# Performance work log

Hardware: AMD Instinct MI355X
Metric: run time of the kernel (lower is better)

## Reference

```python
import jax, jax.numpy as jnp
import numpy as np

GROUPS = 8
HEADS = 8
EPS = 1e-5


def group_norm(x, w, b, groups=GROUPS, eps=EPS):
    # x: [B, C, D, H, W]
    B, C, D, H, W = x.shape
    xg = x.reshape(B, groups, C // groups, D, H, W)
    mu = xg.mean(axis=(2, 3, 4, 5), keepdims=True)
    var = xg.var(axis=(2, 3, 4, 5), keepdims=True)
    xn = ((xg - mu) / jnp.sqrt(var + eps)).reshape(B, C, D, H, W)
    return xn * w[None, :, None, None, None] + b[None, :, None, None, None]


def conv1x1(x, w, b):
    # 1x1x1 Conv3d == channel-mixing GEMM. w: [Cout, Cin], x: [B, Cin, D, H, W]
    y = jnp.einsum('oc,bcdhw->bodhw', w, x)
    return y + b[None, :, None, None, None]


def setup_inputs() -> dict:
    key = jax.random.key(0)
    ks = jax.random.split(key, 8)
    C, CTX = 512, 512
    B, D, H, W = 1, 16, 16, 16
    x = jax.random.normal(ks[0], (B, C, D, H, W), dtype=jnp.float32)
    context = jax.random.normal(ks[1], (B, CTX, D, H, W), dtype=jnp.float32)
    return {
        'x': x,
        'context': context,
        'norm_w': jnp.ones((C,), jnp.float32),
        'norm_b': jnp.zeros((C,), jnp.float32),
        'normc_w': jnp.ones((CTX,), jnp.float32),
        'normc_b': jnp.zeros((CTX,), jnp.float32),
        'q_w': jax.random.normal(ks[2], (C, C), jnp.float32) * 0.02,
        'q_b': jnp.zeros((C,), jnp.float32),
        'kv_w': jax.random.normal(ks[3], (2 * C, CTX), jnp.float32) * 0.02,
        'kv_b': jnp.zeros((2 * C,), jnp.float32),
        'proj_w': jax.random.normal(ks[4], (C, C), jnp.float32) * 0.02,
        'proj_b': jnp.zeros((C,), jnp.float32),
    }


def _split_heads(t, heads):
    # [B, (h c), D, H, W] -> [B, h, S, c] with S = D*H*W
    B, C, D, H, W = t.shape
    return t.reshape(B, heads, C // heads, D * H * W).transpose(0, 1, 3, 2)


def reference(x, context, norm_w, norm_b, normc_w, normc_b,
              q_w, q_b, kv_w, kv_b, proj_w, proj_b):
    B, C, D, H, W = x.shape
    h = group_norm(x, norm_w, norm_b)
    c = group_norm(context, normc_w, normc_b)
    q = conv1x1(h, q_w, q_b)
    kv = conv1x1(c, kv_w, kv_b)
    k, v = jnp.split(kv, 2, axis=1)
    q = _split_heads(q, HEADS)   # [B, h, S, c]
    k = _split_heads(k, HEADS)
    v = _split_heads(v, HEADS)
    scale = (C // HEADS) ** (-0.5)
    logits = jnp.einsum('bhqc,bhkc->bhqk', q, k) * scale
    attn = jax.nn.softmax(logits, axis=-1)
    out = jnp.einsum('bhqk,bhkc->bhqc', attn, v)
    # [B, h, S, c] -> [B, (h c), D, H, W]
    out = out.transpose(0, 1, 3, 2).reshape(B, C, D, H, W)
    out = conv1x1(out, proj_w, proj_b)
    return x + out
```

## Files before the change

### kernel.cpp

```cpp
#include <hip/hip_runtime.h>

typedef unsigned short u16;
typedef unsigned int u32;
typedef float f32x4 __attribute__((ext_vector_type(4)));
typedef __bf16 bf16x8 __attribute__((ext_vector_type(8)));
typedef u32 u32x4 __attribute__((ext_vector_type(4)));
typedef u32 u32x2 __attribute__((ext_vector_type(2)));
typedef short s16x4 __attribute__((ext_vector_type(4)));

#define LOG2E 1.44269504088896340736f

static __device__ __forceinline__ u16 f2bf(float f){ u32 u=__builtin_bit_cast(u32,f); u32 r=u+0x7fffu+((u>>16)&1u); return (u16)(r>>16); }
static __device__ __forceinline__ u32 pk2(float a,float b){ return (u32)f2bf(a)|((u32)f2bf(b)<<16); }
static __device__ __forceinline__ float fexp2(float x){
#if __has_builtin(__builtin_amdgcn_exp2f)
  return __builtin_amdgcn_exp2f(x);
#else
  float r; asm volatile("v_exp_f32 %0, %1" : "=v"(r) : "v"(x)); return r;
#endif
}
static __device__ __forceinline__ f32x4 mfma16(u32x4 a,u32x4 b,f32x4 c){
  return __builtin_amdgcn_mfma_f32_16x16x32_bf16(__builtin_bit_cast(bf16x8,a),__builtin_bit_cast(bf16x8,b),c,0,0,0);
}
#if __has_builtin(__builtin_amdgcn_mfma_f32_16x16x16bf16_1k)
static __device__ __forceinline__ f32x4 mfma1k(s16x4 a,s16x4 b,f32x4 c){
  return __builtin_amdgcn_mfma_f32_16x16x16bf16_1k(a,b,c,0,0,0);
}
#else
static __device__ __forceinline__ f32x4 mfma1k(s16x4 a,s16x4 b,f32x4 c){
  f32x4 d; asm("v_mfma_f32_16x16x16_bf16 %0, %1, %2, %3":"=v"(d):"v"(a),"v"(b),"v"(c)); return d;
}
#endif
static __device__ __forceinline__ u32x4 ldfrag(const u32* p){
  uint2 a=*(const uint2*)p; uint2 b=*(const uint2*)(p+2);
  u32x4 r; r.x=a.x; r.y=a.y; r.z=b.x; r.w=b.y; return r;
}
static __device__ __forceinline__ s16x4 ld8(const u32* p){
  return __builtin_bit_cast(s16x4, *(const u32x2*)p);
}
static __device__ __forceinline__ void stlds(u32* d, uint4 v){
  *(uint2*)d = make_uint2(v.x,v.y); *(uint2*)(d+2) = make_uint2(v.z,v.w);
}
static __device__ __forceinline__ uint4 pack8(float4 a,float4 b){
  uint4 o; o.x=pk2(a.x,a.y); o.y=pk2(a.z,a.w); o.z=pk2(b.x,b.y); o.w=pk2(b.z,b.w); return o;
}

__global__ __launch_bounds__(256) void k_stats(const float* __restrict__ x, const float* __restrict__ c,
                                               float* __restrict__ stats){
  const int g=blockIdx.x>>3, slice=blockIdx.x&7;
  const float* src=(g<8?x:c)+(size_t)(g&7)*262144+(size_t)slice*32768;
  const float4* p=(const float4*)src;
  const int t=threadIdx.x;
  float s1=0.f,s2=0.f;
  for(int i=0;i<32;i++){
    float4 v=p[t+i*256];
    s1+=v.x+v.y+v.z+v.w;
    s2+=v.x*v.x+v.y*v.y+v.z*v.z+v.w*v.w;
  }
  #pragma unroll
  for(int m=1;m<64;m<<=1){ s1+=__shfl_xor(s1,m,64); s2+=__shfl_xor(s2,m,64); }
  __shared__ float r1[4],r2[4];
  const int lane=t&63,w=t>>6;
  if(lane==0){ r1[w]=s1; r2[w]=s2; }
  __syncthreads();
  if(t==0){
    stats[blockIdx.x*2  ]=r1[0]+r1[1]+r1[2]+r1[3];
    stats[blockIdx.x*2+1]=r2[0]+r2[1]+r2[2]+r2[3];
  }
}

__global__ __launch_bounds__(256) void k_qkv(const float* __restrict__ x,const float* __restrict__ ctx,
    const float* __restrict__ qw,const float* __restrict__ qb,
    const float* __restrict__ kvw,const float* __restrict__ kvb,
    const float* __restrict__ nw,const float* __restrict__ nb,
    const float* __restrict__ ncw,const float* __restrict__ ncb,
    const float* __restrict__ stats,
    u16* __restrict__ Qh,u16* __restrict__ Kh,u16* __restrict__ Vp,float qscale){
  __shared__ __align__(16) u32 As[2][64*18];
  __shared__ __align__(16) u32 Bs[2][128*18];
  __shared__ float AB[1024];
  __shared__ float mr[16];
  const int bid=blockIdx.x, t=threadIdx.x, lane=t&63, w=t>>6;
  const int wm=w&1, wn=w>>1, quad=lane>>4, l15=lane&15;
  const bool isV = bid>=512;
  const int z = isV ? 1 : (bid>>8);
  int m0,n0;
  if(isV){ int v=bid-512; n0=(v&31)*128; m0=(v>>5)*64; }
  else   { int r=bid&255; n0=(r&3)*128; m0=(r>>2)*64; }
  const float* anw = z ? ncw : nw;
  const float* anb = z ? ncb : nb;
  if(t<8){
    const int gb = z ? 8 : 0;
    float s1=0.f,s2=0.f;
    #pragma unroll
    for(int s=0;s<8;s++){ s1+=stats[((gb+t)*8+s)*2]; s2+=stats[((gb+t)*8+s)*2+1]; }
    float mean=s1*(1.f/262144.f);
    float var =s2*(1.f/262144.f)-mean*mean;
    mr[t*2]=mean; mr[t*2+1]=rsqrtf(var+1e-5f);
  }
  __syncthreads();
  #pragma unroll
  for(int i=0;i<2;i++){
    int ci=t+i*256, g=ci>>6;
    float al=anw[ci]*mr[g*2+1];
    AB[ci]=al; AB[512+ci]=anb[ci]-mr[g*2]*al;
  }
  __syncthreads();

  const int arow=t>>2, akc=(t&3)*8;
  const int cl=t>>3, s8=(t&7)*8;
  const float* act = z ? ctx : x;
  const float* W   = z ? kvw : qw;
  float4 ta0,ta1,tb0,tb1,tb2,tb3;
  int kpend=0;

  auto loadAB=[&](int kk){
    kpend=kk;
    if(!isV){
      ta0=*(const float4*)(act+(size_t)(kk+cl)*4096+m0+s8);
      ta1=*(const float4*)(act+(size_t)(kk+cl)*4096+m0+s8+4);
      tb0=*(const float4*)(W+(size_t)(n0+arow)*512+kk+akc);
      tb1=*(const float4*)(W+(size_t)(n0+arow)*512+kk+akc+4);
      tb2=*(const float4*)(W+(size_t)(n0+64+arow)*512+kk+akc);
      tb3=*(const float4*)(W+(size_t)(n0+64+arow)*512+kk+akc+4);
    }else{
      ta0=*(const float4*)(kvw+(size_t)(512+m0+arow)*512+kk+akc);
      ta1=*(const float4*)(kvw+(size_t)(512+m0+arow)*512+kk+akc+4);
      tb0=*(const float4*)(ctx+(size_t)(kk+cl)*4096+n0+s8);
      tb1=*(const float4*)(ctx+(size_t)(kk+cl)*4096+n0+s8+4);
      tb2=*(const float4*)(ctx+(size_t)(kk+cl)*4096+n0+64+s8);
      tb3=*(const float4*)(ctx+(size_t)(kk+cl)*4096+n0+64+s8+4);
    }
  };
  auto writeAB=[&](u32* Asb,u32* Bsb){
    if(!isV){
      const float al=AB[kpend+cl], bt=AB[512+kpend+cl];
      float f[8]={ta0.x,ta0.y,ta0.z,ta0.w,ta1.x,ta1.y,ta1.z,ta1.w};
      u16* As16=(u16*)Asb;
      #pragma unroll
      for(int j=0;j<8;j++) As16[(s8+j)*36+cl]=f2bf(al*f[j]+bt);
      stlds(&Bsb[arow*18+(akc>>1)],pack8(tb0,tb1));
      stlds(&Bsb[(64+arow)*18+(akc>>1)],pack8(tb2,tb3));
    }else{
      stlds(&Asb[arow*18+(akc>>1)],pack8(ta0,ta1));
      const float al=AB[kpend+cl], bt=AB[512+kpend+cl];
      float f[8]={tb0.x,tb0.y,tb0.z,tb0.w,tb1.x,tb1.y,tb1.z,tb1.w};
      float g[8]={tb2.x,tb2.y,tb2.z,tb2.w,tb3.x,tb3.y,tb3.z,tb3.w};
      u16* Bs16=(u16*)Bsb;
      #pragma unroll
      for(int j=0;j<8;j++){
        Bs16[(s8+j)*36+cl]=f2bf(al*f[j]+bt);
        Bs16[(64+s8+j)*36+cl]=f2bf(al*g[j]+bt);
      }
    }
  };

  f32x4 acc[2][4];
  #pragma unroll
  for(int i=0;i<2;i++)
    #pragma unroll
    for(int j=0;j<4;j++){ acc[i][j].x=0.f; acc[i][j].y=0.f; acc[i][j].z=0.f; acc[i][j].w=0.f; }

  auto compute=[&](const u32* Asb,const u32* Bsb){
    const u32* Ab=Asb+(wm*32+l15)*18+quad*4;
    const u32* Bb=Bsb+(wn*64+l15)*18+quad*4;
    u32x4 af[2], bfr[4];
    #pragma unroll
    for(int mt=0;mt<2;mt++) af[mt]=ldfrag(Ab+mt*288);
    #pragma unroll
    for(int nt=0;nt<4;nt++) bfr[nt]=ldfrag(Bb+nt*288);
    #pragma unroll
    for(int mt=0;mt<2;mt++)
      #pragma unroll
      for(int nt=0;nt<4;nt++) acc[mt][nt]=mfma16(af[mt],bfr[nt],acc[mt][nt]);
  };

  loadAB(0); writeAB(As[0],Bs[0]);
  __syncthreads();
  for(int kk=0;kk<512;kk+=64){
    loadAB(kk+32);
    compute(As[0],Bs[0]);
    writeAB(As[1],Bs[1]);
    __syncthreads();
    const bool n2=(kk+64)<512;
    if(n2) loadAB(kk+64);
    compute(As[1],Bs[1]);
    if(n2){ writeAB(As[0],Bs[0]); __syncthreads(); }
  }
  #pragma unroll
  for(int mt=0;mt<2;mt++)
    #pragma unroll
    for(int nt=0;nt<4;nt++){
      const int n = n0 + wn*64 + nt*16 + l15;
      if(!isV){
        u16* out = z ? Kh : Qh;
        const float scale = z ? 1.f : qscale;
        const float bn = (z ? kvb[n] : qb[n]);
        const size_t base = ((size_t)((n>>6)*4096))*64 + (size_t)(n&63);
        #pragma unroll
        for(int r=0;r<4;r++){
          int m = m0 + wm*32 + mt*16 + quad*4 + r;
          out[base + (size_t)m*64] = f2bf((acc[mt][nt][r]+bn)*scale);
        }
      } else {
        #pragma unroll
        for(int r=0;r<4;r++){
          int m = m0 + wm*32 + mt*16 + quad*4 + r;
          Vp[(size_t)m*4096+n] = f2bf(acc[mt][nt][r] + kvb[512+m]);
        }
      }
    }
}

__global__ __launch_bounds__(256) void k_proj(const float* __restrict__ A,const u16* __restrict__ B,
    const float* __restrict__ bias,const float* __restrict__ residf,float* __restrict__ out){
  __shared__ __align__(16) u32 As[2][64*18];
  __shared__ __align__(16) u32 Bs[2][128*18];
  const int t=threadIdx.x, lane=t&63, w=t>>6;
  const int wm=w&1, wn=w>>1, quad=lane>>4, l15=lane&15;
  const int m0=blockIdx.y*64, n0=blockIdx.x*128;
  const int arow=t>>2, akc=(t&3)*8;
  float4 ra0,ra1; uint4 rb0,rb1;
  auto loadAB=[&](int kk){
    ra0=*(const float4*)(A+(size_t)(m0+arow)*512+kk+akc);
    ra1=*(const float4*)(A+(size_t)(m0+arow)*512+kk+akc+4);
    rb0=*(const uint4*)(B+((size_t)((kk>>6)*4096+n0+arow))*64+(kk&63)+akc);
    rb1=*(const uint4*)(B+((size_t)((kk>>6)*4096+n0+64+arow))*64+(kk&63)+akc);
  };
  auto writeAB=[&](u32* Asb,u32* Bsb){
    stlds(&Asb[arow*18+(akc>>1)],pack8(ra0,ra1));
    stlds(&Bsb[arow*18+(akc>>1)],rb0);
    stlds(&Bsb[(64+arow)*18+(akc>>1)],rb1);
  };
  f32x4 acc[2][4];
  #pragma unroll
  for(int i=0;i<2;i++)
    #pragma unroll
    for(int j=0;j<4;j++){ acc[i][j].x=0.f; acc[i][j].y=0.f; acc[i][j].z=0.f; acc[i][j].w=0.f; }
  auto compute=[&](const u32* Asb,const u32* Bsb){
    const u32* Ab=Asb+(wm*32+l15)*18+quad*4;
    const u32* Bb=Bsb+(wn*64+l15)*18+quad*4;
    u32x4 af[2], bfr[4];
    #pragma unroll
    for(int mt=0;mt<2;mt++) af[mt]=ldfrag(Ab+mt*288);
    #pragma unroll
    for(int nt=0;nt<4;nt++) bfr[nt]=ldfrag(Bb+nt*288);
    #pragma unroll
    for(int mt=0;mt<2;mt++)
      #pragma unroll
      for(int nt=0;nt<4;nt++) acc[mt][nt]=mfma16(af[mt],bfr[nt],acc[mt][nt]);
  };
  loadAB(0); writeAB(As[0],Bs[0]);
  __syncthreads();
  for(int kk=0;kk<512;kk+=64){
    loadAB(kk+32);
    compute(As[0],Bs[0]);
    writeAB(As[1],Bs[1]);
    __syncthreads();
    const bool n2=(kk+64)<512;
    if(n2) loadAB(kk+64);
    compute(As[1],Bs[1]);
    if(n2){ writeAB(As[0],Bs[0]); __syncthreads(); }
  }
  #pragma unroll
  for(int mt=0;mt<2;mt++)
    #pragma unroll
    for(int nt=0;nt<4;nt++){
      const int n = n0 + wn*64 + nt*16 + l15;
      #pragma unroll
      for(int r=0;r<4;r++){
        int m = m0 + wm*32 + mt*16 + quad*4 + r;
        out[(size_t)m*4096+n] = acc[mt][nt][r] + bias[m] + residf[(size_t)m*4096+n];
      }
    }
}

__global__ __launch_bounds__(512,4) void k_attn(const u16* __restrict__ Qh,const u16* __restrict__ Kh,
                                              const u16* __restrict__ Vp,u16* __restrict__ Oh){
  __shared__ __align__(16) u32 KS[2][2][64*34];
  __shared__ __align__(16) u32 VS[2][2][64*34];
  const int t=threadIdx.x, lane=t&63, w=t>>6, quad=lane>>4, l15=lane&15;
  const int half=w>>2, wq=w&3;
  const int h=blockIdx.y, s0=blockIdx.x*64;
  const int tt=t&255, srow=tt>>2, sc=(tt&3)*16;
  const u16* Kg = Kh + ((size_t)(h*4096 + half*2048 + srow))*64 + sc;
  const u16* Vg = Vp + (size_t)(h*64+srow)*4096 + half*2048 + sc;
  const u32* Qg = (const u32*)(Qh + ((size_t)(h*4096+s0+wq*16+l15))*64);
  u32x4 qfw[2];
  qfw[0]=ldfrag(Qg + quad*4);
  qfw[1]=ldfrag(Qg + 16 + quad*4);

  uint4 pk0,pk1,pv0,pv1;
  auto loadKV=[&](int t0l){
    const u16* kp=Kg+(size_t)t0l*64;
    pk0=*(const uint4*)kp; pk1=*(const uint4*)(kp+8);
    const u16* vp=Vg+t0l;
    pv0=*(const uint4*)vp; pv1=*(const uint4*)(vp+8);
  };
  auto writeKV=[&](u32* Kb,u32* Vb){
    u32* kw=Kb+srow*34+(sc>>1);
    stlds(kw,pk0); stlds(kw+4,pk1);
    u32* vw=Vb+srow*34+(sc>>1);
    stlds(vw,pv0); stlds(vw+4,pv1);
  };

  float lrun=0.f; f32x4 oacc[4];
  #pragma unroll
  for(int cn=0;cn<4;cn++){ oacc[cn].x=0.f; oacc[cn].y=0.f; oacc[cn].z=0.f; oacc[cn].w=0.f; }

  auto tilestep=[&](const u32* Kb,const u32* Vb){
    f32x4 sv[4];
    #pragma unroll
    for(int nt=0;nt<4;nt++){
      const u32* kb=Kb+(nt*16+l15)*34+quad*4;
      f32x4 a; a.x=0.f; a.y=0.f; a.z=0.f; a.w=0.f;
      a=mfma16(ldfrag(kb),qfw[0],a);
      a=mfma16(ldfrag(kb+16),qfw[1],a);
      sv[nt]=a;
    }
    s16x4 pfr[4];
    #pragma unroll
    for(int nt=0;nt<4;nt++){
      float p0=fexp2(sv[nt].x),p1=fexp2(sv[nt].y),p2=fexp2(sv[nt].z),p3=fexp2(sv[nt].w);
      lrun+=(p0+p1)+(p2+p3);
      u32x2 pp;
      pp.x=(__builtin_bit_cast(u32,p0)>>16)|(__builtin_bit_cast(u32,p1)&0xffff0000u);
      pp.y=(__builtin_bit_cast(u32,p2)>>16)|(__builtin_bit_cast(u32,p3)&0xffff0000u);
      pfr[nt]=__builtin_bit_cast(s16x4,pp);
    }
    #pragma unroll
    for(int cn=0;cn<4;cn++){
      const u32* vb=Vb+(cn*16+l15)*34+quad*2;
      f32x4 a=oacc[cn];
      #pragma unroll
      for(int nt=0;nt<4;nt++) a=mfma1k(pfr[nt],ld8(vb+nt*8),a);
      oacc[cn]=a;
    }
  };

  loadKV(0); writeKV(KS[half][0],VS[half][0]);
  __syncthreads();
  for(int t0=0;t0<2048;t0+=128){
    loadKV(t0+64);
    tilestep(KS[half][0],VS[half][0]);
    writeKV(KS[half][1],VS[half][1]);
    __syncthreads();
    const bool more=(t0+128)<2048;
    if(more) loadKV(t0+128);
    tilestep(KS[half][1],VS[half][1]);
    if(more){ writeKV(KS[half][0],VS[half][0]); __syncthreads(); }
  }
  __syncthreads();
  float* cb=(float*)KS[1];
  const int cbi=(wq*64+lane)*17;
  if(half==1){
    #pragma unroll
    for(int cn=0;cn<4;cn++)
      #pragma unroll
      for(int r=0;r<4;r++) cb[cbi+cn*4+r]=oacc[cn][r];
    cb[cbi+16]=lrun;
  }
  __syncthreads();
  if(half==0){
    #pragma unroll
    for(int cn=0;cn<4;cn++)
      #pragma unroll
      for(int r=0;r<4;r++) oacc[cn][r]+=cb[cbi+cn*4+r];
    lrun+=cb[cbi+16];
    float l=lrun;
    l+=__shfl_xor(l,16,64);
    l+=__shfl_xor(l,32,64);
    #pragma unroll
    for(int r=0;r<4;r++){
      float inv=1.f/__shfl(l,quad*4+r,64);
      #pragma unroll
      for(int cn=0;cn<4;cn++)
        Oh[((size_t)(h*4096+s0+wq*16+quad*4+r))*64 + cn*16 + l15]=f2bf(oacc[cn][r]*inv);
    }
  }
}

extern "C" void kernel_launch(void* const* d_in, const int* in_sizes, int n_in,
                              void* d_out, int out_size, void* d_ws, size_t ws_size,
                              hipStream_t stream){
  (void)in_sizes; (void)n_in; (void)out_size; (void)ws_size;
  const float* x  =(const float*)d_in[0];
  const float* ctx=(const float*)d_in[1];
  const float* nw =(const float*)d_in[2];
  const float* nb =(const float*)d_in[3];
  const float* ncw=(const float*)d_in[4];
  const float* ncb=(const float*)d_in[5];
  const float* qw =(const float*)d_in[6];
  const float* qb =(const float*)d_in[7];
  const float* kvw=(const float*)d_in[8];
  const float* kvb=(const float*)d_in[9];
  const float* pw =(const float*)d_in[10];
  const float* pb =(const float*)d_in[11];
  float* out=(float*)d_out;
  char* ws=(char*)d_ws;
  float* stats=(float*)ws;
  u16* Qh  =(u16*)(ws+16384);
  u16* Kh  =(u16*)(ws+16384+4194304);
  u16* Vp  =(u16*)(ws+16384+2*4194304);
  u16* Oh  =(u16*)(ws+16384+3*4194304);

  k_stats<<<dim3(128),dim3(256),0,stream>>>(x,ctx,stats);
  k_qkv<<<dim3(768),dim3(256),0,stream>>>(x,ctx,qw,qb,kvw,kvb,nw,nb,ncw,ncb,stats,Qh,Kh,Vp,0.125f*LOG2E);
  k_attn<<<dim3(64,8),dim3(512),0,stream>>>(Qh,Kh,Vp,Oh);
  k_proj<<<dim3(32,8),dim3(256),0,stream>>>(pw,Oh,pb,x,out);
}
```

Baseline: 176.4 us.

## Pre-normalize and transpose inputs to bf16, unify GEMMs, widen attention Q tile

A new k_norm kernel applies the group-norm affine, casts to bf16, transposes activations to a sequence-major layout, and pre-converts all weights to bf16. This replaces the fused normalize-in-GEMM loaders with one templated bf16 GEMM using 128x128 tiles and 16-byte LDS fragment loads. The attention kernel now processes two Q tiles per block so each K/V fragment is reused twice, and uses a new LDS padding. Weights are converted again on every call, and the extra launch plus workspace aliasing add traffic and ordering risk.

After: 187.6 us. 1.06x slower.

```diff
diff --git a/kernel.cpp b/kernel.cpp
--- a/kernel.cpp
+++ b/kernel.cpp
@@ -31,10 +31,7 @@
   f32x4 d; asm("v_mfma_f32_16x16x16_bf16 %0, %1, %2, %3":"=v"(d):"v"(a),"v"(b),"v"(c)); return d;
 }
 #endif
-static __device__ __forceinline__ u32x4 ldfrag(const u32* p){
-  uint2 a=*(const uint2*)p; uint2 b=*(const uint2*)(p+2);
-  u32x4 r; r.x=a.x; r.y=a.y; r.z=b.x; r.w=b.y; return r;
-}
+static __device__ __forceinline__ u32x4 ld16(const u32* p){ return *(const u32x4*)p; }
 static __device__ __forceinline__ s16x4 ld8(const u32* p){
   return __builtin_bit_cast(s16x4, *(const u32x2*)p);
 }
@@ -47,8 +44,8 @@
 
 __global__ __launch_bounds__(256) void k_stats(const float* __restrict__ x, const float* __restrict__ c,
                                                float* __restrict__ stats){
-  const int g=blockIdx.x>>3, slice=blockIdx.x&7;
-  const float* src=(g<8?x:c)+(size_t)(g&7)*262144+(size_t)slice*32768;
+  const int g=blockIdx.x>>3;
+  const float* src=(g<8?x:c)+(size_t)(g&7)*262144+(size_t)(blockIdx.x&7)*32768;
   const float4* p=(const float4*)src;
   const int t=threadIdx.x;
   float s1=0.f,s2=0.f;
@@ -69,227 +66,185 @@
   }
 }
 
-__global__ __launch_bounds__(256) void k_qkv(const float* __restrict__ x,const float* __restrict__ ctx,
-    const float* __restrict__ qw,const float* __restrict__ qb,
-    const float* __restrict__ kvw,const float* __restrict__ kvb,
+__global__ __launch_bounds__(256) void k_norm(const float* __restrict__ x,const float* __restrict__ ctx,
+    const float* __restrict__ qw,const float* __restrict__ kvw,const float* __restrict__ pw,
     const float* __restrict__ nw,const float* __restrict__ nb,
     const float* __restrict__ ncw,const float* __restrict__ ncb,
     const float* __restrict__ stats,
-    u16* __restrict__ Qh,u16* __restrict__ Kh,u16* __restrict__ Vp,float qscale){
-  __shared__ __align__(16) u32 As[2][64*18];
-  __shared__ __align__(16) u32 Bs[2][128*18];
-  __shared__ float AB[1024];
-  __shared__ float mr[16];
-  const int bid=blockIdx.x, t=threadIdx.x, lane=t&63, w=t>>6;
-  const int wm=w&1, wn=w>>1, quad=lane>>4, l15=lane&15;
-  const bool isV = bid>=512;
-  const int z = isV ? 1 : (bid>>8);
-  int m0,n0;
-  if(isV){ int v=bid-512; n0=(v&31)*128; m0=(v>>5)*64; }
-  else   { int r=bid&255; n0=(r&3)*128; m0=(r>>2)*64; }
-  const float* anw = z ? ncw : nw;
-  const float* anb = z ? ncb : nb;
-  if(t<8){
-    const int gb = z ? 8 : 0;
+    u16* __restrict__ xnT,u16* __restrict__ cnT,u16* __restrict__ Wall){
+  const int bid=blockIdx.x, t=threadIdx.x;
+  if(bid>=256){
+    const int wb=bid-256;
+    const float* src = wb<8 ? pw+(size_t)wb*32768 : (wb<16 ? qw+(size_t)(wb-8)*32768 : kvw+(size_t)(wb-16)*32768);
+    u16* dst = Wall + (size_t)wb*32768;
+    #pragma unroll
+    for(int it=0;it<16;it++){
+      int off = it*2048 + t*8;
+      float4 a=*(const float4*)(src+off), b=*(const float4*)(src+off+4);
+      *(uint4*)(dst+off) = pack8(a,b);
+    }
+    return;
+  }
+  const int op=bid>>7, r=bid&127;
+  const int c0=(r>>4)*64, s0=(r&15)*256;
+  const float* src = op? ctx : x;
+  u16* dst = op? cnT : xnT;
+  const float* anw = op? ncw : nw;
+  const float* anb = op? ncb : nb;
+  __shared__ float al[64], bt[64];
+  __shared__ u32 T[256*37];
+  if(t<64){
+    int c=c0+t, g=(op?8:0)+(c>>6);
     float s1=0.f,s2=0.f;
     #pragma unroll
-    for(int s=0;s<8;s++){ s1+=stats[((gb+t)*8+s)*2]; s2+=stats[((gb+t)*8+s)*2+1]; }
+    for(int s=0;s<8;s++){ s1+=stats[(g*8+s)*2]; s2+=stats[(g*8+s)*2+1]; }
     float mean=s1*(1.f/262144.f);
     float var =s2*(1.f/262144.f)-mean*mean;
-    mr[t*2]=mean; mr[t*2+1]=rsqrtf(var+1e-5f);
-  }
-  __syncthreads();
-  #pragma unroll
-  for(int i=0;i<2;i++){
-    int ci=t+i*256, g=ci>>6;
-    float al=anw[ci]*mr[g*2+1];
-    AB[ci]=al; AB[512+ci]=anb[ci]-mr[g*2]*al;
-  }
-  __syncthreads();
-
-  const int arow=t>>2, akc=(t&3)*8;
-  const int cl=t>>3, s8=(t&7)*8;
-  const float* act = z ? ctx : x;
-  const float* W   = z ? kvw : qw;
-  float4 ta0,ta1,tb0,tb1,tb2,tb3;
-  int kpend=0;
-
+    float a=anw[c]*rsqrtf(var+1e-5f);
+    al[t]=a; bt[t]=anb[c]-mean*a;
+  }
+  __syncthreads();
+  const int pr=t>>3, sj=(t&7)*8;
+  const float a0=al[2*pr], b0=bt[2*pr], a1=al[2*pr+1], b1=bt[2*pr+1];
+  #pragma unroll
+  for(int it=0;it<4;it++){
+    int ls=it*64+sj;
+    const float* p0=src+(size_t)(c0+2*pr)*4096+s0+ls;
+    const float* p1=src+(size_t)(c0+2*pr+1)*4096+s0+ls;
+    float4 va=*(const float4*)p0, vb=*(const float4*)(p0+4);
+    float4 vc=*(const float4*)p1, vd=*(const float4*)(p1+4);
+    float f0[8]={va.x,va.y,va.z,va.w,vb.x,vb.y,vb.z,vb.w};
+    float f1[8]={vc.x,vc.y,vc.z,vc.w,vd.x,vd.y,vd.z,vd.w};
+    #pragma unroll
+    for(int j=0;j<8;j++)
+      T[(ls+j)*37+pr]=pk2(a0*f0[j]+b0, a1*f1[j]+b1);
+  }
+  __syncthreads();
+  #pragma unroll
+  for(int ps=0;ps<8;ps++){
+    int row = ps*32 + (t>>3);
+    const u32* rp=&T[row*37+(t&7)*4];
+    u32 v0=rp[0],v1=rp[1],v2=rp[2],v3=rp[3];
+    *(uint4*)(dst + (size_t)(s0+row)*512 + c0 + (t&7)*8) = make_uint4(v0,v1,v2,v3);
+  }
+}
+
+template<int EPI,int BG,int ZS>
+__global__ __launch_bounds__(256,2) void k_gemm(const u16* __restrict__ A0,const u16* __restrict__ A1,
+    const u16* __restrict__ B0,const u16* __restrict__ B1,
+    const float* __restrict__ bias0,const float* __restrict__ bias1,
+    const float* __restrict__ residf,void* __restrict__ out0,void* __restrict__ out1,
+    float scale0,float scale1){
+  __shared__ __align__(16) u32 As[2][128*20];
+  __shared__ __align__(16) u32 Bs[2][128*20];
+  const int t=threadIdx.x, lane=t&63, w=t>>6;
+  const int wm=w&1, wn=w>>1, quad=lane>>4, l15=lane&15;
+  const int bid=blockIdx.x;
+  const int z = ZS ? (bid>>7) : 0;
+  const int r = ZS ? (bid&127) : bid;
+  const u16* A = z? A1:A0;
+  const u16* B = z? B1:B0;
+  const float* bias = z? bias1:bias0;
+  void* outv = z? out1:out0;
+  const float scale = z? scale1:scale0;
+  int m0,n0;
+  if(EPI==0){ m0=(r>>2)*128; n0=(r&3)*128; }
+  else      { m0=(r>>5)*128; n0=(r&31)*128; }
+  const int arow=t>>1, ak=(t&1)*16;
+  uint4 a0,a1,b0,b1;
   auto loadAB=[&](int kk){
-    kpend=kk;
-    if(!isV){
-      ta0=*(const float4*)(act+(size_t)(kk+cl)*4096+m0+s8);
-      ta1=*(const float4*)(act+(size_t)(kk+cl)*4096+m0+s8+4);
-      tb0=*(const float4*)(W+(size_t)(n0+arow)*512+kk+akc);
-      tb1=*(const float4*)(W+(size_t)(n0+arow)*512+kk+akc+4);
-      tb2=*(const float4*)(W+(size_t)(n0+64+arow)*512+kk+akc);
-      tb3=*(const float4*)(W+(size_t)(n0+64+arow)*512+kk+akc+4);
-    }else{
-      ta0=*(const float4*)(kvw+(size_t)(512+m0+arow)*512+kk+akc);
-      ta1=*(const float4*)(kvw+(size_t)(512+m0+arow)*512+kk+akc+4);
-      tb0=*(const float4*)(ctx+(size_t)(kk+cl)*4096+n0+s8);
-      tb1=*(const float4*)(ctx+(size_t)(kk+cl)*4096+n0+s8+4);
-      tb2=*(const float4*)(ctx+(size_t)(kk+cl)*4096+n0+64+s8);
-      tb3=*(const float4*)(ctx+(size_t)(kk+cl)*4096+n0+64+s8+4);
-    }
-  };
-  auto writeAB=[&](u32* Asb,u32* Bsb){
-    if(!isV){
-      const float al=AB[kpend+cl], bt=AB[512+kpend+cl];
-      float f[8]={ta0.x,ta0.y,ta0.z,ta0.w,ta1.x,ta1.y,ta1.z,ta1.w};
-      u16* As16=(u16*)Asb;
-      #pragma unroll
-      for(int j=0;j<8;j++) As16[(s8+j)*36+cl]=f2bf(al*f[j]+bt);
-      stlds(&Bsb[arow*18+(akc>>1)],pack8(tb0,tb1));
-      stlds(&Bsb[(64+arow)*18+(akc>>1)],pack8(tb2,tb3));
-    }else{
-      stlds(&Asb[arow*18+(akc>>1)],pack8(ta0,ta1));
-      const float al=AB[kpend+cl], bt=AB[512+kpend+cl];
-      float f[8]={tb0.x,tb0.y,tb0.z,tb0.w,tb1.x,tb1.y,tb1.z,tb1.w};
-      float g[8]={tb2.x,tb2.y,tb2.z,tb2.w,tb3.x,tb3.y,tb3.z,tb3.w};
-      u16* Bs16=(u16*)Bsb;
-      #pragma unroll
-      for(int j=0;j<8;j++){
-        Bs16[(s8+j)*36+cl]=f2bf(al*f[j]+bt);
-        Bs16[(64+s8+j)*36+cl]=f2bf(al*g[j]+bt);
-      }
-    }
-  };
-
-  f32x4 acc[2][4];
-  #pragma unroll
-  for(int i=0;i<2;i++)
+    const u16* ap=A+(size_t)(m0+arow)*512+kk+ak;
+    a0=*(const uint4*)ap; a1=*(const uint4*)(ap+8);
+    const u16* bp;
+    if(BG) bp = B + ((size_t)((kk>>6)*4096 + n0+arow))*64 + (kk&63) + ak;
+    else   bp = B + (size_t)(n0+arow)*512 + kk + ak;
+    b0=*(const uint4*)bp; b1=*(const uint4*)(bp+8);
+  };
+  auto writeAB=[&](int bsel){
+    u32* aw=&As[bsel][arow*20+(ak>>1)];
+    stlds(aw,a0); stlds(aw+4,a1);
+    u32* bw=&Bs[bsel][arow*20+(ak>>1)];
+    stlds(bw,b0); stlds(bw+4,b1);
+  };
+  f32x4 acc[4][4];
+  #pragma unroll
+  for(int i=0;i<4;i++)
     #pragma unroll
     for(int j=0;j<4;j++){ acc[i][j].x=0.f; acc[i][j].y=0.f; acc[i][j].z=0.f; acc[i][j].w=0.f; }
-
-  auto compute=[&](const u32* Asb,const u32* Bsb){
-    const u32* Ab=Asb+(wm*32+l15)*18+quad*4;
-    const u32* Bb=Bsb+(wn*64+l15)*18+quad*4;
-    u32x4 af[2], bfr[4];
-    #pragma unroll
-    for(int mt=0;mt<2;mt++) af[mt]=ldfrag(Ab+mt*288);
-    #pragma unroll
-    for(int nt=0;nt<4;nt++) bfr[nt]=ldfrag(Bb+nt*288);
-    #pragma unroll
-    for(int mt=0;mt<2;mt++)
-      #pragma unroll
-      for(int nt=0;nt<4;nt++) acc[mt][nt]=mfma16(af[mt],bfr[nt],acc[mt][nt]);
-  };
-
-  loadAB(0); writeAB(As[0],Bs[0]);
+  auto compute=[&](int bsel){
+    const u32* Ab=&As[bsel][(wm*64+l15)*20+quad*4];
+    const u32* Bb=&Bs[bsel][(wn*64+l15)*20+quad*4];
+    u32x4 af[4], bf[4];
+    #pragma unroll
+    for(int mt=0;mt<4;mt++) af[mt]=ld16(Ab+mt*320);
+    #pragma unroll
+    for(int nt=0;nt<4;nt++) bf[nt]=ld16(Bb+nt*320);
+    #pragma unroll
+    for(int mt=0;mt<4;mt++)
+      #pragma unroll
+      for(int nt=0;nt<4;nt++) acc[mt][nt]=mfma16(af[mt],bf[nt],acc[mt][nt]);
+  };
+  loadAB(0); writeAB(0);
   __syncthreads();
   for(int kk=0;kk<512;kk+=64){
     loadAB(kk+32);
-    compute(As[0],Bs[0]);
-    writeAB(As[1],Bs[1]);
+    compute(0);
+    writeAB(1);
     __syncthreads();
     const bool n2=(kk+64)<512;
     if(n2) loadAB(kk+64);
-    compute(As[1],Bs[1]);
-    if(n2){ writeAB(As[0],Bs[0]); __syncthreads(); }
-  }
-  #pragma unroll
-  for(int mt=0;mt<2;mt++)
+    compute(1);
+    if(n2){ writeAB(0); __syncthreads(); }
+  }
+  #pragma unroll
+  for(int mt=0;mt<4;mt++)
     #pragma unroll
     for(int nt=0;nt<4;nt++){
       const int n = n0 + wn*64 + nt*16 + l15;
-      if(!isV){
-        u16* out = z ? Kh : Qh;
-        const float scale = z ? 1.f : qscale;
-        const float bn = (z ? kvb[n] : qb[n]);
-        const size_t base = ((size_t)((n>>6)*4096))*64 + (size_t)(n&63);
-        #pragma unroll
-        for(int r=0;r<4;r++){
-          int m = m0 + wm*32 + mt*16 + quad*4 + r;
-          out[base + (size_t)m*64] = f2bf((acc[mt][nt][r]+bn)*scale);
+      if(EPI==0){
+        u16* out=(u16*)outv;
+        const float bn=bias[n];
+        const size_t base=((size_t)((n>>6)*4096))*64+(size_t)(n&63);
+        #pragma unroll
+        for(int r4=0;r4<4;r4++){
+          int m=m0+wm*64+mt*16+quad*4+r4;
+          out[base+(size_t)m*64]=f2bf((acc[mt][nt][r4]+bn)*scale);
         }
-      } else {
-        #pragma unroll
-        for(int r=0;r<4;r++){
-          int m = m0 + wm*32 + mt*16 + quad*4 + r;
-          Vp[(size_t)m*4096+n] = f2bf(acc[mt][nt][r] + kvb[512+m]);
+      }else if(EPI==1){
+        u16* out=(u16*)outv;
+        #pragma unroll
+        for(int r4=0;r4<4;r4++){
+          int m=m0+wm*64+mt*16+quad*4+r4;
+          out[(size_t)m*4096+n]=f2bf(acc[mt][nt][r4]+bias[m]);
         }
-      }
-    }
-}
-
-__global__ __launch_bounds__(256) void k_proj(const float* __restrict__ A,const u16* __restrict__ B,
-    const float* __restrict__ bias,const float* __restrict__ residf,float* __restrict__ out){
-  __shared__ __align__(16) u32 As[2][64*18];
-  __shared__ __align__(16) u32 Bs[2][128*18];
-  const int t=threadIdx.x, lane=t&63, w=t>>6;
-  const int wm=w&1, wn=w>>1, quad=lane>>4, l15=lane&15;
-  const int m0=blockIdx.y*64, n0=blockIdx.x*128;
-  const int arow=t>>2, akc=(t&3)*8;
-  float4 ra0,ra1; uint4 rb0,rb1;
-  auto loadAB=[&](int kk){
-    ra0=*(const float4*)(A+(size_t)(m0+arow)*512+kk+akc);
-    ra1=*(const float4*)(A+(size_t)(m0+arow)*512+kk+akc+4);
-    rb0=*(const uint4*)(B+((size_t)((kk>>6)*4096+n0+arow))*64+(kk&63)+akc);
-    rb1=*(const uint4*)(B+((size_t)((kk>>6)*4096+n0+64+arow))*64+(kk&63)+akc);
-  };
-  auto writeAB=[&](u32* Asb,u32* Bsb){
-    stlds(&Asb[arow*18+(akc>>1)],pack8(ra0,ra1));
-    stlds(&Bsb[arow*18+(akc>>1)],rb0);
-    stlds(&Bsb[(64+arow)*18+(akc>>1)],rb1);
-  };
-  f32x4 acc[2][4];
-  #pragma unroll
-  for(int i=0;i<2;i++)
-    #pragma unroll
-    for(int j=0;j<4;j++){ acc[i][j].x=0.f; acc[i][j].y=0.f; acc[i][j].z=0.f; acc[i][j].w=0.f; }
-  auto compute=[&](const u32* Asb,const u32* Bsb){
-    const u32* Ab=Asb+(wm*32+l15)*18+quad*4;
-    const u32* Bb=Bsb+(wn*64+l15)*18+quad*4;
-    u32x4 af[2], bfr[4];
-    #pragma unroll
-    for(int mt=0;mt<2;mt++) af[mt]=ldfrag(Ab+mt*288);
-    #pragma unroll
-    for(int nt=0;nt<4;nt++) bfr[nt]=ldfrag(Bb+nt*288);
-    #pragma unroll
-    for(int mt=0;mt<2;mt++)
-      #pragma unroll
-      for(int nt=0;nt<4;nt++) acc[mt][nt]=mfma16(af[mt],bfr[nt],acc[mt][nt]);
-  };
-  loadAB(0); writeAB(As[0],Bs[0]);
-  __syncthreads();
-  for(int kk=0;kk<512;kk+=64){
-    loadAB(kk+32);
-    compute(As[0],Bs[0]);
-    writeAB(As[1],Bs[1]);
-    __syncthreads();
-    const bool n2=(kk+64)<512;
-    if(n2) loadAB(kk+64);
-    compute(As[1],Bs[1]);
-    if(n2){ writeAB(As[0],Bs[0]); __syncthreads(); }
-  }
-  #pragma unroll
-  for(int mt=0;mt<2;mt++)
-    #pragma unroll
-    for(int nt=0;nt<4;nt++){
-      const int n = n0 + wn*64 + nt*16 + l15;
-      #pragma unroll
-      for(int r=0;r<4;r++){
-        int m = m0 + wm*32 + mt*16 + quad*4 + r;
-        out[(size_t)m*4096+n] = acc[mt][nt][r] + bias[m] + residf[(size_t)m*4096+n];
-      }
-    }
-}
-
-__global__ __launch_bounds__(512,4) void k_attn(const u16* __restrict__ Qh,const u16* __restrict__ Kh,
+      }else{
+        float* out=(float*)outv;
+        #pragma unroll
+        for(int r4=0;r4<4;r4++){
+          int m=m0+wm*64+mt*16+quad*4+r4;
+          out[(size_t)m*4096+n]=acc[mt][nt][r4]+bias[m]+residf[(size_t)m*4096+n];
+        }
+      }
+    }
+}
+
+__global__ __launch_bounds__(512) void k_attn(const u16* __restrict__ Qh,const u16* __restrict__ Kh,
                                               const u16* __restrict__ Vp,u16* __restrict__ Oh){
-  __shared__ __align__(16) u32 KS[2][2][64*34];
-  __shared__ __align__(16) u32 VS[2][2][64*34];
+  __shared__ __align__(16) u32 KS[2][2][64*36];
+  __shared__ __align__(16) u32 VS[2][2][64*36];
   const int t=threadIdx.x, lane=t&63, w=t>>6, quad=lane>>4, l15=lane&15;
   const int half=w>>2, wq=w&3;
-  const int h=blockIdx.y, s0=blockIdx.x*64;
+  const int h=blockIdx.y, q0=blockIdx.x*128;
   const int tt=t&255, srow=tt>>2, sc=(tt&3)*16;
   const u16* Kg = Kh + ((size_t)(h*4096 + half*2048 + srow))*64 + sc;
   const u16* Vg = Vp + (size_t)(h*64+srow)*4096 + half*2048 + sc;
-  const u32* Qg = (const u32*)(Qh + ((size_t)(h*4096+s0+wq*16+l15))*64);
-  u32x4 qfw[2];
-  qfw[0]=ldfrag(Qg + quad*4);
-  qfw[1]=ldfrag(Qg + 16 + quad*4);
-
+  u32x4 qf[2][2];
+  #pragma unroll
+  for(int qt=0;qt<2;qt++){
+    const u32* Qg=(const u32*)(Qh + ((size_t)(h*4096+q0+qt*64+wq*16+l15))*64);
+    qf[qt][0]=ld16(Qg+quad*4);
+    qf[qt][1]=ld16(Qg+16+quad*4);
+  }
   uint4 pk0,pk1,pv0,pv1;
   auto loadKV=[&](int t0l){
     const u16* kp=Kg+(size_t)t0l*64;
@@ -298,43 +253,54 @@
     pv0=*(const uint4*)vp; pv1=*(const uint4*)(vp+8);
   };
   auto writeKV=[&](u32* Kb,u32* Vb){
-    u32* kw=Kb+srow*34+(sc>>1);
+    u32* kw=Kb+srow*36+(sc>>1);
     stlds(kw,pk0); stlds(kw+4,pk1);
-    u32* vw=Vb+srow*34+(sc>>1);
+    u32* vw=Vb+srow*36+(sc>>1);
     stlds(vw,pv0); stlds(vw+4,pv1);
   };
-
-  float lrun=0.f; f32x4 oacc[4];
-  #pragma unroll
-  for(int cn=0;cn<4;cn++){ oacc[cn].x=0.f; oacc[cn].y=0.f; oacc[cn].z=0.f; oacc[cn].w=0.f; }
+  float lrun[2]={0.f,0.f};
+  f32x4 oacc[2][4];
+  #pragma unroll
+  for(int qt=0;qt<2;qt++)
+    #pragma unroll
+    for(int cn=0;cn<4;cn++){ oacc[qt][cn].x=0.f; oacc[qt][cn].y=0.f; oacc[qt][cn].z=0.f; oacc[qt][cn].w=0.f; }
 
   auto tilestep=[&](const u32* Kb,const u32* Vb){
-    f32x4 sv[4];
+    f32x4 sv[2][4];
     #pragma unroll
     for(int nt=0;nt<4;nt++){
-      const u32* kb=Kb+(nt*16+l15)*34+quad*4;
-      f32x4 a; a.x=0.f; a.y=0.f; a.z=0.f; a.w=0.f;
-      a=mfma16(ldfrag(kb),qfw[0],a);
-      a=mfma16(ldfrag(kb+16),qfw[1],a);
-      sv[nt]=a;
-    }
-    s16x4 pfr[4];
-    #pragma unroll
-    for(int nt=0;nt<4;nt++){
-      float p0=fexp2(sv[nt].x),p1=fexp2(sv[nt].y),p2=fexp2(sv[nt].z),p3=fexp2(sv[nt].w);
-      lrun+=(p0+p1)+(p2+p3);
-      u32x2 pp;
-      pp.x=(__builtin_bit_cast(u32,p0)>>16)|(__builtin_bit_cast(u32,p1)&0xffff0000u);
-      pp.y=(__builtin_bit_cast(u32,p2)>>16)|(__builtin_bit_cast(u32,p3)&0xffff0000u);
-      pfr[nt]=__builtin_bit_cast(s16x4,pp);
-    }
+      const u32* kb=Kb+(nt*16+l15)*36+quad*4;
+      u32x4 k0=ld16(kb), k1=ld16(kb+16);
+      #pragma unroll
+      for(int qt=0;qt<2;qt++){
+        f32x4 a; a.x=0.f; a.y=0.f; a.z=0.f; a.w=0.f;
+        a=mfma16(k0,qf[qt][0],a);
+        sv[qt][nt]=mfma16(k1,qf[qt][1],a);
+      }
+    }
+    s16x4 pfr[2][4];
+    #pragma unroll
+    for(int qt=0;qt<2;qt++)
+      #pragma unroll
+      for(int nt=0;nt<4;nt++){
+        float p0=fexp2(sv[qt][nt].x),p1=fexp2(sv[qt][nt].y),p2=fexp2(sv[qt][nt].z),p3=fexp2(sv[qt][nt].w);
+        lrun[qt]+=(p0+p1)+(p2+p3);
+        u32x2 pp;
+        pp.x=(__builtin_bit_cast(u32,p0)>>16)|(__builtin_bit_cast(u32,p1)&0xffff0000u);
+        pp.y=(__builtin_bit_cast(u32,p2)>>16)|(__builtin_bit_cast(u32,p3)&0xffff0000u);
+        pfr[qt][nt]=__builtin_bit_cast(s16x4,pp);
+      }
     #pragma unroll
     for(int cn=0;cn<4;cn++){
-      const u32* vb=Vb+(cn*16+l15)*34+quad*2;
-      f32x4 a=oacc[cn];
-      #pragma unroll
-      for(int nt=0;nt<4;nt++) a=mfma1k(pfr[nt],ld8(vb+nt*8),a);
-      oacc[cn]=a;
+      const u32* vb=Vb+(cn*16+l15)*36+quad*2;
+      f32x4 a0=oacc[0][cn], a1=oacc[1][cn];
+      #pragma unroll
+      for(int nt=0;nt<4;nt++){
+        s16x4 vf=ld8(vb+nt*8);
+        a0=mfma1k(pfr[0][nt],vf,a0);
+        a1=mfma1k(pfr[1][nt],vf,a1);
+      }
+      oacc[0][cn]=a0; oacc[1][cn]=a1;
     }
   };
 
@@ -351,31 +317,35 @@
     if(more){ writeKV(KS[half][0],VS[half][0]); __syncthreads(); }
   }
   __syncthreads();
-  float* cb=(float*)KS[1];
-  const int cbi=(wq*64+lane)*17;
+  float* cb=(float*)KS;
+  const int cbi=(wq*64+lane)*34;
   if(half==1){
     #pragma unroll
-    for(int cn=0;cn<4;cn++)
-      #pragma unroll
-      for(int r=0;r<4;r++) cb[cbi+cn*4+r]=oacc[cn][r];
-    cb[cbi+16]=lrun;
+    for(int qt=0;qt<2;qt++)
+      #pragma unroll
+      for(int cn=0;cn<4;cn++)
+        #pragma unroll
+        for(int r4=0;r4<4;r4++) cb[cbi+qt*16+cn*4+r4]=oacc[qt][cn][r4];
+    cb[cbi+32]=lrun[0]; cb[cbi+33]=lrun[1];
   }
   __syncthreads();
   if(half==0){
     #pragma unroll
-    for(int cn=0;cn<4;cn++)
-      #pragma unroll
-      for(int r=0;r<4;r++) oacc[cn][r]+=cb[cbi+cn*4+r];
-    lrun+=cb[cbi+16];
-    float l=lrun;
-    l+=__shfl_xor(l,16,64);
-    l+=__shfl_xor(l,32,64);
-    #pragma unroll
-    for(int r=0;r<4;r++){
-      float inv=1.f/__shfl(l,quad*4+r,64);
+    for(int qt=0;qt<2;qt++){
       #pragma unroll
       for(int cn=0;cn<4;cn++)
-        Oh[((size_t)(h*4096+s0+wq*16+quad*4+r))*64 + cn*16 + l15]=f2bf(oacc[cn][r]*inv);
+        #pragma unroll
+        for(int r4=0;r4<4;r4++) oacc[qt][cn][r4]+=cb[cbi+qt*16+cn*4+r4];
+      float l=lrun[qt]+cb[cbi+32+qt];
+      l+=__shfl_xor(l,16,64);
+      l+=__shfl_xor(l,32,64);
+      #pragma unroll
+      for(int r4=0;r4<4;r4++){
+        float inv=1.f/__shfl(l,quad*4+r4,64);
+        #pragma unroll
+        for(int cn=0;cn<4;cn++)
+          Oh[((size_t)(h*4096+q0+qt*64+wq*16+quad*4+r4))*64 + cn*16 + l15]=f2bf(oacc[qt][cn][r4]*inv);
+      }
     }
   }
 }
@@ -399,13 +369,22 @@
   float* out=(float*)d_out;
   char* ws=(char*)d_ws;
   float* stats=(float*)ws;
-  u16* Qh  =(u16*)(ws+16384);
-  u16* Kh  =(u16*)(ws+16384+4194304);
-  u16* Vp  =(u16*)(ws+16384+2*4194304);
-  u16* Oh  =(u16*)(ws+16384+3*4194304);
+  u16* Wall=(u16*)(ws+1024);
+  u16* pwb  = Wall;
+  u16* qwb  = Wall+262144;
+  u16* kvw1b= Wall+524288;
+  u16* kvw2b= Wall+786432;
+  u16* cnT=(u16*)(ws+2098176);
+  u16* xnT=(u16*)(ws+6292480);
+  u16* Qh =(u16*)(ws+10486784);
+  u16* Kh =(u16*)(ws+14681088);
+  u16* Vp =(u16*)(ws+6292480);
+  u16* Oh =(u16*)(ws+2098176);
 
   k_stats<<<dim3(128),dim3(256),0,stream>>>(x,ctx,stats);
-  k_qkv<<<dim3(768),dim3(256),0,stream>>>(x,ctx,qw,qb,kvw,kvb,nw,nb,ncw,ncb,stats,Qh,Kh,Vp,0.125f*LOG2E);
-  k_attn<<<dim3(64,8),dim3(512),0,stream>>>(Qh,Kh,Vp,Oh);
-  k_proj<<<dim3(32,8),dim3(256),0,stream>>>(pw,Oh,pb,x,out);
-}
+  k_norm<<<dim3(288),dim3(256),0,stream>>>(x,ctx,qw,kvw,pw,nw,nb,ncw,ncb,stats,xnT,cnT,Wall);
+  k_gemm<0,0,1><<<dim3(256),dim3(256),0,stream>>>(xnT,cnT,qwb,kvw1b,qb,kvb,nullptr,Qh,Kh,0.125f*LOG2E,1.f);
+  k_gemm<1,0,0><<<dim3(128),dim3(256),0,stream>>>(kvw2b,nullptr,cnT,nullptr,kvb+512,nullptr,nullptr,Vp,nullptr,1.f,1.f);
+  k_attn<<<dim3(32,8),dim3(512),0,stream>>>(Qh,Kh,Vp,Oh);
+  k_gemm<2,1,0><<<dim3(128),dim3(256),0,stream>>>(pwb,nullptr,Oh,nullptr,pb,nullptr,x,out,nullptr,1.f,1.f);
+}
```
